# Kernel optimization log

Hardware: AMD Instinct MI355X
Metric: run time of the kernel (lower is better)

## Reference

```python
import jax, jax.numpy as jnp
import numpy as np

FEAT_STRIDE = 16
NEG_OV, POS_OV = 0.3, 0.7
RPN_BATCH = 256
NUM_FG = int(0.5 * RPN_BATCH)  # RPN_FG_FRACTION * RPN_BATCHSIZE


def _gen_anchors(base=16, ratios=(0.5, 1.0, 2.0), scales=(4, 8, 16)):
    # 3D extension of the classic generate_anchors: ratio warps w/h, scale multiplies all dims
    ctr = (base - 1) / 2.0
    rows = []
    for r in ratios:
        for s in scales:
            w = base * s * np.sqrt(1.0 / r)
            h = base * s * np.sqrt(r)
            d = float(base * s)
            rows.append([ctr - 0.5 * (w - 1), ctr - 0.5 * (h - 1),
                         ctr + 0.5 * (w - 1), ctr + 0.5 * (h - 1),
                         ctr - 0.5 * (d - 1), ctr + 0.5 * (d - 1)])
    return np.asarray(rows, np.float32)


def setup_inputs() -> dict:
    key = jax.random.key(0)
    ks = jax.random.split(key, 8)
    B, H, W, D, K, A = 2, 48, 48, 24, 20, 9
    cls = jax.random.normal(ks[0], (B, 2 * A, H, W, D), jnp.float32)
    x1 = jax.random.uniform(ks[1], (B, K)) * 600.0
    y1 = jax.random.uniform(ks[2], (B, K)) * 600.0
    z1 = jax.random.uniform(ks[3], (B, K)) * 300.0
    whd = 16.0 + jax.random.uniform(ks[4], (B, K, 3)) * jnp.array([104.0, 104.0, 48.0])
    x2 = jnp.minimum(x1 + whd[..., 0], 767.0)
    y2 = jnp.minimum(y1 + whd[..., 1], 767.0)
    z2 = jnp.minimum(z1 + whd[..., 2], 383.0)
    cid = jax.random.randint(ks[5], (B, K), 1, 4).astype(jnp.float32)
    gt_boxes = jnp.stack([x1, y1, x2, y2, z1, z2, cid], axis=2)
    im_info = jnp.tile(jnp.array([[768.0, 768.0, 384.0]], jnp.float32), (B, 1))
    total = H * W * D * A
    return {
        'rpn_cls_score': cls,
        'gt_boxes': gt_boxes,
        'im_info': im_info,
        'num_boxes': jnp.full((B,), K, jnp.int32),
        'anchors': jnp.asarray(_gen_anchors()),
        'rand_fg': jax.random.uniform(ks[6], (B, total)),
        'rand_bg': jax.random.uniform(ks[7], (B, total)),
    }


def _overlaps(anc, gt):
    # anc: (N,6) [x1,y1,x2,y2,z1,z2]; gt: (B,K,7) -> IoU (B,N,K)
    aw = anc[:, 2] - anc[:, 0] + 1.0
    ah = anc[:, 3] - anc[:, 1] + 1.0
    ad = anc[:, 5] - anc[:, 4] + 1.0
    a_area = aw * ah * ad  # (N,)
    gw = gt[:, :, 2] - gt[:, :, 0] + 1.0
    gh = gt[:, :, 3] - gt[:, :, 1] + 1.0
    gd = gt[:, :, 5] - gt[:, :, 4] + 1.0
    g_area = gw * gh * gd  # (B,K)
    iw = jnp.clip(jnp.minimum(anc[None, :, None, 2], gt[:, None, :, 2]) -
                  jnp.maximum(anc[None, :, None, 0], gt[:, None, :, 0]) + 1.0, 0.0)
    ih = jnp.clip(jnp.minimum(anc[None, :, None, 3], gt[:, None, :, 3]) -
                  jnp.maximum(anc[None, :, None, 1], gt[:, None, :, 1]) + 1.0, 0.0)
    idp = jnp.clip(jnp.minimum(anc[None, :, None, 5], gt[:, None, :, 5]) -
                   jnp.maximum(anc[None, :, None, 4], gt[:, None, :, 4]) + 1.0, 0.0)
    inter = iw * ih * idp
    ov = inter / (a_area[None, :, None] + g_area[:, None, :] - inter)
    gt_zero = (gw == 1.0) & (gh == 1.0) & (gd == 1.0)
    a_zero = (aw == 1.0) & (ah == 1.0) & (ad == 1.0)
    ov = jnp.where(gt_zero[:, None, :], 0.0, ov)
    ov = jnp.where(a_zero[None, :, None], -1.0, ov)
    return ov


def _transform(ex, gt):
    # ex: (N,6); gt: (B,N,6) -> (B,N,6) targets (dx,dy,dz,dw,dh,dd)
    ew = ex[:, 2] - ex[:, 0] + 1.0
    eh = ex[:, 3] - ex[:, 1] + 1.0
    ed = ex[:, 5] - ex[:, 4] + 1.0
    ecx = ex[:, 0] + 0.5 * (ew - 1.0)
    ecy = ex[:, 1] + 0.5 * (eh - 1.0)
    ecz = ex[:, 4] + 0.5 * (ed - 1.0)
    gw = gt[:, :, 2] - gt[:, :, 0] + 1.0
    gh = gt[:, :, 3] - gt[:, :, 1] + 1.0
    gd = gt[:, :, 5] - gt[:, :, 4] + 1.0
    gcx = gt[:, :, 0] + 0.5 * (gw - 1.0)
    gcy = gt[:, :, 1] + 0.5 * (gh - 1.0)
    gcz = gt[:, :, 4] + 0.5 * (gd - 1.0)
    return jnp.stack([(gcx - ecx[None]) / ew[None],
                      (gcy - ecy[None]) / eh[None],
                      (gcz - ecz[None]) / ed[None],
                      jnp.log(gw / ew[None]),
                      jnp.log(gh / eh[None]),
                      jnp.log(gd / ed[None])], axis=2)


def _rank(p):
    # rank of each element when sorted by descending priority, per row
    return jnp.argsort(jnp.argsort(-p, axis=1), axis=1)


def reference(rpn_cls_score, gt_boxes, im_info, num_boxes, anchors, rand_fg, rand_bg):
    B = gt_boxes.shape[0]
    H, W, D = rpn_cls_score.shape[2], rpn_cls_score.shape[3], rpn_cls_score.shape[4]
    A = anchors.shape[0]
    sx = jnp.arange(W, dtype=jnp.float32) * FEAT_STRIDE
    sy = jnp.arange(H, dtype=jnp.float32) * FEAT_STRIDE
    sz = jnp.arange(D, dtype=jnp.float32) * FEAT_STRIDE
    mx, my, mz = jnp.meshgrid(sx, sy, sz, indexing='xy')  # (H,W,D) each
    shifts = jnp.stack([mx.ravel(), my.ravel(), mx.ravel(), my.ravel(), mz.ravel(), mz.ravel()], axis=1)
    all_anchors = (anchors[None, :, :] + shifts[:, None, :]).reshape(-1, 6)  # (total,6)
    total = all_anchors.shape[0]
    inside = ((all_anchors[:, 0] >= 0) & (all_anchors[:, 1] >= 0) & (all_anchors[:, 4] >= 0) &
              (all_anchors[:, 2] < im_info[0, 1]) & (all_anchors[:, 3] < im_info[0, 0]) &
              (all_anchors[:, 5] < im_info[0, 2]))  # (total,)

    ov = _overlaps(all_anchors, gt_boxes)                       # (B,total,K)
    ov_m = jnp.where(inside[None, :, None], ov, -1.0)           # mask outside anchors
    max_ov = ov_m.max(axis=2)
    argmax_ov = jnp.argmax(ov_m, axis=2)                        # (B,total)

    labels = jnp.full((B, total), -1.0, jnp.float32)
    ins = inside[None, :]
    labels = jnp.where(ins & (max_ov < NEG_OV), 0.0, labels)
    gt_max = ov_m.max(axis=1)                                   # (B,K)
    gt_max = jnp.where(gt_max == 0.0, 1e-5, gt_max)
    tie = jnp.sum(ov_m == gt_max[:, None, :], axis=2) > 0
    labels = jnp.where(ins & tie, 1.0, labels)
    labels = jnp.where(ins & (max_ov >= POS_OV), 1.0, labels)

    # fg subsampling: randomly keep at most NUM_FG positives per image
    fg = labels == 1.0
    rk = _rank(jnp.where(fg, rand_fg, -1.0))
    labels = jnp.where(fg & (rk >= NUM_FG), -1.0, labels)
    # bg subsampling: keep RPN_BATCH - num_fg negatives per image
    num_bg = RPN_BATCH - jnp.sum(labels == 1.0, axis=1)         # (B,)
    bg = labels == 0.0
    rkb = _rank(jnp.where(bg, rand_bg, -1.0))
    labels = jnp.where(bg & (rkb >= num_bg[:, None]), -1.0, labels)

    assigned = jnp.take_along_axis(gt_boxes, argmax_ov[:, :, None], axis=1)  # (B,total,7)
    bbox_targets = _transform(all_anchors, assigned[:, :, :6])
    bbox_targets = jnp.where(inside[None, :, None], bbox_targets, 0.0)

    in_w = jnp.where(labels == 1.0, 1.0, 0.0)                   # RPN_BBOX_INSIDE_WEIGHTS[0]=1
    # replicate original bug: weights from the LAST image's example count
    num_examples = jnp.sum(labels[-1] >= 0.0).astype(jnp.float32)
    w = 1.0 / num_examples
    out_w = jnp.where(labels == 1.0, w, jnp.where(labels == 0.0, w, 0.0))

    labels_o = labels.reshape(B, H, W, D, A).transpose(0, 4, 1, 2, 3).reshape(B, 1, A * H * D, W)
    bt_o = bbox_targets.reshape(B, H, W, D, A * 6).transpose(0, 4, 1, 2, 3)
    iw_o = jnp.broadcast_to(in_w[:, :, None], (B, total, 6)).reshape(B, H, W, D, 6 * A).transpose(0, 4, 1, 2, 3)
    ow_o = jnp.broadcast_to(out_w[:, :, None], (B, total, 6)).reshape(B, H, W, D, 6 * A).transpose(0, 4, 1, 2, 3)
    return labels_o, bt_o, iw_o, ow_o
```

## Files before the change

kernel.cpp:

```cpp
#include <hip/hip_runtime.h>
#include <math.h>

#define BB 2
#define HH 48
#define WW 48
#define DD 24
#define KK 20
#define AA 9
#define TOTAL (HH*WW*DD*AA)
#define SPAT (HH*WW*DD)
#define OUT0N (BB*TOTAL)
#define CH 54
#define NB 4096
#define CAPB 256
#define FG_QUOTA 128
#define RPN_B 256
#define STRIDE_F 16.0f
#define K1_SB 54
#define NPART (AA*K1_SB)

#define O_REC    0
#define O_GTMAX  (OUT0N)
#define O_HIST   (O_GTMAX + BB*KK)
#define O_CUT    (O_HIST + 4*NB)
#define O_W      (O_CUT + 16)
#define O_LIST   (O_W + 1)
#define O_PART   (O_LIST + 4*NB*CAPB)

struct GtRec { float x1,y1,x2,y2,z1,z2,area; };
__device__ __forceinline__ GtRec gt_load(const float* __restrict__ gt, int b, int k){
  #pragma clang fp contract(off)
  const float* p = &gt[(b*KK+k)*7];
  GtRec g;
  g.x1=p[0]; g.y1=p[1]; g.x2=p[2]; g.y2=p[3]; g.z1=p[4]; g.z2=p[5];
  float gw = g.x2-g.x1+1.0f, gh = g.y2-g.y1+1.0f, gd = g.z2-g.z1+1.0f;
  g.area = gw*gh*gd;
  return g;
}

__device__ __forceinline__ float iou_rec(float ax1,float ay1,float ax2,float ay2,
                                         float az1,float az2,float a_area,
                                         const GtRec& g){
  #pragma clang fp contract(off)
  float iw = fminf(ax2,g.x2) - fmaxf(ax1,g.x1) + 1.0f; iw = fmaxf(iw,0.0f);
  float ih = fminf(ay2,g.y2) - fmaxf(ay1,g.y1) + 1.0f; ih = fmaxf(ih,0.0f);
  float id = fminf(az2,g.z2) - fmaxf(az1,g.z1) + 1.0f; id = fmaxf(id,0.0f);
  float inter = iw*ih*id;
  if (inter <= 0.0f) return 0.0f;
  return inter / ((a_area + g.area) - inter);
}

__global__ void __launch_bounds__(256) k_gtmax(const float* __restrict__ gt,
    const float* __restrict__ anc, const float* __restrict__ imi,
    unsigned* __restrict__ ws){
  float* ws_f = (float*)ws;
  __shared__ float s_red[4][KK];
  int tid = threadIdx.x;
  int wv = tid>>6, ln = tid&63;
  int a = blockIdx.y, b = blockIdx.z;
  if (b==0 && a==0 && blockIdx.x<16){
    int base = blockIdx.x*256 + tid;
    #pragma unroll
    for (int j=0;j<4;j++) ws[O_HIST + j*NB + base] = 0u;
  }
  float im0=imi[0], im1=imi[1], im2=imi[2];
  float a0=anc[a*6+0], a1=anc[a*6+1], a2=anc[a*6+2];
  float a3=anc[a*6+3], a4=anc[a*6+4], a5=anc[a*6+5];
  int s0 = blockIdx.x*256 + tid;
  float X1[4],Y1[4],X2[4],Y2[4],Z1[4],Z2[4],AR[4];
  bool OK[4];
  #pragma unroll
  for (int j=0;j<4;j++){
    int s = s0 + j*(K1_SB*256);
    int d = s % DD; int s2 = s/DD; int w = s2%WW; int h = s2/WW;
    float fx=w*STRIDE_F, fy=h*STRIDE_F, fz=d*STRIDE_F;
    X1[j]=a0+fx; Y1[j]=a1+fy; X2[j]=a2+fx; Y2[j]=a3+fy; Z1[j]=a4+fz; Z2[j]=a5+fz;
    OK[j] = (X1[j]>=0.f)&&(Y1[j]>=0.f)&&(Z1[j]>=0.f)&&
            (X2[j]<im1)&&(Y2[j]<im0)&&(Z2[j]<im2);
    {
      #pragma clang fp contract(off)
      float aw=X2[j]-X1[j]+1.0f, ah=Y2[j]-Y1[j]+1.0f, ad=Z2[j]-Z1[j]+1.0f;
      AR[j]=aw*ah*ad;
    }
  }
  #pragma unroll
  for (int k=0;k<KK;k++){
    GtRec g = gt_load(gt,b,k);
    float m = -1.0f;
    #pragma unroll
    for (int j=0;j<4;j++)
      if (OK[j]) m = fmaxf(m, iou_rec(X1[j],Y1[j],X2[j],Y2[j],Z1[j],Z2[j],AR[j],g));
    #pragma unroll
    for (int off=32; off>0; off>>=1) m = fmaxf(m, __shfl_down(m, off, 64));
    if (ln==0) s_red[wv][k]=m;
  }
  __syncthreads();
  if (tid<KK){
    float m = fmaxf(fmaxf(s_red[0][tid],s_red[1][tid]),
                    fmaxf(s_red[2][tid],s_red[3][tid]));
    ws_f[O_PART + (b*KK+tid)*NPART + a*K1_SB + blockIdx.x] = m;
  }
}

__global__ void __launch_bounds__(256) k_label(const float* __restrict__ gt,
    const float* __restrict__ anc, const float* __restrict__ imi,
    const float* __restrict__ rfg, const float* __restrict__ rbg,
    unsigned* __restrict__ ws){
  float* ws_f = (float*)ws;
  __shared__ float s_gm[KK];
  int tid = threadIdx.x;
  int blk = blockIdx.x;
  int wv = tid>>6, ln = tid&63;
  int t4 = (blk*256 + tid)*4;
  int d0 = t4 % DD; int r1=t4/DD; int w=r1%WW; int r2=r1/WW; int h=r2%HH;
  int b = blk/486; int a = (blk%486)/54;
  int ibase = ((h*WW+w)*DD + d0)*AA + a;
  float rfv[4], rbv[4];
  #pragma unroll
  for (int dd=0;dd<4;dd++){
    rfv[dd] = rfg[b*TOTAL + ibase + dd*AA];
    rbv[dd] = rbg[b*TOTAL + ibase + dd*AA];
  }
  for (int k=wv; k<KK; k+=4){
    float m = -1.0f;
    for (int j=ln; j<NPART; j+=64)
      m = fmaxf(m, ws_f[O_PART + (b*KK+k)*NPART + j]);
    #pragma unroll
    for (int off=32; off>0; off>>=1) m = fmaxf(m, __shfl_down(m, off, 64));
    if (ln==0){ if (m==0.0f) m = 1e-5f; s_gm[k]=m; }
  }
  __syncthreads();
  float im0=imi[0], im1=imi[1], im2=imi[2];
  float a0=anc[a*6+0], a1=anc[a*6+1], a2=anc[a*6+2];
  float a3=anc[a*6+3], a4=anc[a*6+4], a5=anc[a*6+5];
  float fx=w*STRIDE_F, fy=h*STRIDE_F;
  float ax1=a0+fx, ay1=a1+fy, ax2=a2+fx, ay2=a3+fy;
  bool okxy = (ax1>=0.f)&&(ay1>=0.f)&&(ax2<im1)&&(ay2<im0);
  float Z1[4],Z2[4],AR[4]; bool OK[4];
  #pragma unroll
  for (int dd=0;dd<4;dd++){
    float fz = (float)(d0+dd)*STRIDE_F;
    Z1[dd]=a4+fz; Z2[dd]=a5+fz;
    OK[dd] = okxy && (Z1[dd]>=0.f) && (Z2[dd]<im2);
    {
      #pragma clang fp contract(off)
      float aw=ax2-ax1+1.0f, ah=ay2-ay1+1.0f, ad=Z2[dd]-Z1[dd]+1.0f;
      AR[dd]=aw*ah*ad;
    }
  }
  float mv[4]={-2.f,-2.f,-2.f,-2.f};
  int   am[4]={0,0,0,0};
  bool  tie[4]={false,false,false,false};
  #pragma unroll
  for (int k=0;k<KK;k++){
    GtRec g = gt_load(gt,b,k);
    float gmk = s_gm[k];
    #pragma unroll
    for (int dd=0;dd<4;dd++){
      if (OK[dd]){
        float ov = iou_rec(ax1,ay1,ax2,ay2,Z1[dd],Z2[dd],AR[dd],g);
        if (ov > mv[dd]){ mv[dd]=ov; am[dd]=k; }
        tie[dd] = tie[dd] || (ov == gmk);
      }
    }
  }
  unsigned recs[4];
  #pragma unroll
  for (int dd=0;dd<4;dd++){
    float L = -1.0f;
    if (OK[dd]){
      if (mv[dd] < 0.3f) L = 0.0f;
      if (tie[dd])       L = 1.0f;
      if (mv[dd] >= 0.7f) L = 1.0f;
    }
    unsigned code = (L==1.0f) ? 2u : ((L==0.0f) ? 1u : 0u);
    unsigned bucket = 0;
    if (code){
      int fl = (code==1u ? 2 : 0) + b;
      float r = (code==1u) ? rbv[dd] : rfv[dd];
      bucket = (unsigned)min(NB-1, (int)(r*(float)NB));
      unsigned pos = atomicAdd(&ws[O_HIST + fl*NB + bucket], 1u);
      if (pos < CAPB) ((int*)ws)[O_LIST + ((fl*NB + (int)bucket)<<8) + pos] = ibase + dd*AA;
    }
    recs[dd] = code | ((unsigned)am[dd]<<2) | (bucket<<7);
  }
  *reinterpret_cast<uint4*>(&ws[O_REC + t4]) = make_uint4(recs[0],recs[1],recs[2],recs[3]);
}

__global__ void __launch_bounds__(256) k_cuts(unsigned* __restrict__ ws){
  int fl = blockIdx.x; int tid = threadIdx.x;
  int b = fl & 1; int isbg = fl >> 1;
  const int CHK = NB/256;
  __shared__ unsigned ps[256];
  __shared__ unsigned s_fg;
  if (tid == 0) s_fg = 0u;
  __syncthreads();
  int hi = NB - CHK*tid;
  unsigned hv[16];
  #pragma unroll
  for (int e=0; e<CHK; e++) hv[e] = ws[O_HIST + fl*NB + (hi-CHK+e)];
  unsigned part = 0;
  #pragma unroll
  for (int e=0; e<CHK; e++) part += hv[e];
  if (isbg){
    unsigned pf = 0;
    #pragma unroll
    for (int e=0; e<CHK; e++) pf += ws[O_HIST + b*NB + tid*CHK + e];
    atomicAdd(&s_fg, pf);
  }
  ps[tid] = part;
  __syncthreads();
  for (int off=1; off<256; off<<=1){
    unsigned v = (tid>=off) ? ps[tid-off] : 0u;
    __syncthreads();
    ps[tid] += v;
    __syncthreads();
  }
  unsigned N = ps[255];
  unsigned excl = ps[tid] - part;
  unsigned F = isbg ? s_fg : N;
  int quota = isbg ? (RPN_B - (int)min(F, (unsigned)FG_QUOTA)) : FG_QUOTA;
  if (fl == 3 && tid == 0){
    int fgk = min((int)F, FG_QUOTA);
    int bgk = min((int)N, RPN_B - fgk);
    ((float*)ws)[O_W] = 1.0f / (float)(fgk + bgk);
  }
  int* cut = (int*)&ws[O_CUT + fl*4];
  if ((int)N <= quota){
    if (tid==0){ cut[0] = -1; cut[1] = 0; cut[2] = quota; cut[3] = 0; }
    return;
  }
  unsigned cum = excl;
  #pragma unroll
  for (int e=CHK-1; e>=0; e--){
    int bk = hi-CHK+e;
    unsigned c = hv[e];
    if (c > 0u && (unsigned)(quota-1) >= cum && (unsigned)(quota-1) < cum + c){
      cut[0] = bk; cut[1] = (int)cum; cut[2] = quota; cut[3] = (int)c;
    }
    cum += c;
  }
}

__global__ void __launch_bounds__(256) k_out(const float* __restrict__ gt,
    const float* __restrict__ anc, const float* __restrict__ imi,
    const float* __restrict__ rfg, const float* __restrict__ rbg,
    float* __restrict__ out, const unsigned* __restrict__ ws){
  __shared__ float s_gt[BB*KK*7];
  __shared__ float s_anc[AA*6];
  __shared__ float s_im[3];
  __shared__ float s_w;
  int tid = threadIdx.x;
  for (int j=tid; j<BB*KK*7; j+=256) s_gt[j] = gt[j];
  for (int j=tid; j<AA*6; j+=256) s_anc[j] = anc[j];
  if (tid<3) s_im[tid] = imi[tid];
  if (tid==0) s_w = ((const float*)ws)[O_W];
  __syncthreads();
  int t4 = (blockIdx.x*256 + tid)*4;
  int d0 = t4 % DD; int r1=t4/DD;
  int w = r1 % WW; int r2 = r1/WW;
  int h = r2 % HH; int r3 = r2/HH;
  int a = r3 % AA; int b = r3/AA;
  const uint4 rec4 = *reinterpret_cast<const uint4*>(&ws[O_REC + t4]);
  unsigned recs[4] = {rec4.x, rec4.y, rec4.z, rec4.w};
  float sw = s_w;
  float fx=w*STRIDE_F, fy=h*STRIDE_F;
  float ax1=s_anc[a*6+0]+fx, ay1=s_anc[a*6+1]+fy;
  float ax2=s_anc[a*6+2]+fx, ay2=s_anc[a*6+3]+fy;
  float L4[4], iw4[4], ow4[4], btv[6][4];
  #pragma unroll
  for (int dd=0; dd<4; dd++){
    int d = d0 + dd;
    unsigned rec = recs[dd];
    unsigned code = rec & 3u;
    int am = (int)((rec>>2) & 31u);
    int bucket = (int)((rec>>7) & 4095u);
    float L = (code==2u) ? 1.0f : ((code==1u) ? 0.0f : -1.0f);
    if (code){
      int isbg = (code==1u);
      int fl = isbg*2 + b;
      const int* cut = (const int*)&ws[O_CUT + fl*4];
      int cutb = cut[0];
      if (cutb >= 0){
        if (bucket < cutb) L = -1.0f;
        else if (bucket == cutb){
          int rank_base = cut[1], quota = cut[2];
          int n = min(cut[3], CAPB);
          int i = ((h*WW+w)*DD + d)*AA + a;
          const float* ra = isbg ? rbg : rfg;
          float ri = ra[b*TOTAL + i];
          const int* lst = (const int*)ws + O_LIST + ((fl*NB + cutb)<<8);
          int cnt = 0;
          for (int e=0; e<n; e++){
            int jj = lst[e];
            float rj = ra[b*TOTAL + jj];
            cnt += (rj > ri) || (rj == ri && jj < i);
          }
          if (rank_base + cnt >= quota) L = -1.0f;
        }
      }
    }
    float fz = d*STRIDE_F;
    float az1 = s_anc[a*6+4]+fz, az2 = s_anc[a*6+5]+fz;
    bool inside = (ax1>=0.f)&&(ay1>=0.f)&&(az1>=0.f)&&
                  (ax2<s_im[1])&&(ay2<s_im[0])&&(az2<s_im[2]);
    float bt[6] = {0.f,0.f,0.f,0.f,0.f,0.f};
    if (inside){
      const float* g = &s_gt[(b*KK + am)*7];
      float ew=ax2-ax1+1.f, eh=ay2-ay1+1.f, ed=az2-az1+1.f;
      float ecx=ax1+0.5f*(ew-1.f), ecy=ay1+0.5f*(eh-1.f), ecz=az1+0.5f*(ed-1.f);
      float gw=g[2]-g[0]+1.f, gh=g[3]-g[1]+1.f, gd=g[5]-g[4]+1.f;
      float gcx=g[0]+0.5f*(gw-1.f), gcy=g[1]+0.5f*(gh-1.f), gcz=g[4]+0.5f*(gd-1.f);
      bt[0]=(gcx-ecx)/ew; bt[1]=(gcy-ecy)/eh; bt[2]=(gcz-ecz)/ed;
      bt[3]=logf(gw/ew);  bt[4]=logf(gh/eh);  bt[5]=logf(gd/ed);
    }
    L4[dd] = L;
    iw4[dd] = (L==1.0f) ? 1.0f : 0.0f;
    ow4[dd] = (L==1.0f || L==0.0f) ? sw : 0.0f;
    #pragma unroll
    for (int c=0; c<6; c++) btv[c][dd] = bt[c];
  }
  *reinterpret_cast<float4*>(&out[t4]) = make_float4(L4[0],L4[1],L4[2],L4[3]);
  int sp = (h*WW + w)*DD + d0;
  float* out1 = out + OUT0N;
  float* out2 = out1 + BB*CH*SPAT;
  float* out3 = out2 + BB*CH*SPAT;
  int basech = (b*CH + a*6)*SPAT + sp;
  float4 iwv = make_float4(iw4[0],iw4[1],iw4[2],iw4[3]);
  float4 owv = make_float4(ow4[0],ow4[1],ow4[2],ow4[3]);
  #pragma unroll
  for (int c=0; c<6; c++){
    int off = basech + c*SPAT;
    *reinterpret_cast<float4*>(&out1[off]) = make_float4(btv[c][0],btv[c][1],btv[c][2],btv[c][3]);
    *reinterpret_cast<float4*>(&out2[off]) = iwv;
    *reinterpret_cast<float4*>(&out3[off]) = owv;
  }
}

extern "C" void kernel_launch(void* const* d_in, const int* in_sizes, int n_in,
                              void* d_out, int out_size, void* d_ws, size_t ws_size,
                              hipStream_t stream) {
  (void)in_sizes; (void)n_in; (void)out_size; (void)ws_size;
  const float* gt  = (const float*)d_in[1];
  const float* imi = (const float*)d_in[2];
  const float* anc = (const float*)d_in[4];
  const float* rfg = (const float*)d_in[5];
  const float* rbg = (const float*)d_in[6];
  float* out = (float*)d_out;
  unsigned* ws = (unsigned*)d_ws;
  int nb4 = (OUT0N + 1023)/1024;
  k_gtmax <<<dim3(K1_SB, AA, BB), dim3(256), 0, stream>>>(gt, anc, imi, ws);
  k_label <<<dim3(nb4), dim3(256), 0, stream>>>(gt, anc, imi, rfg, rbg, ws);
  k_cuts  <<<dim3(4), dim3(256), 0, stream>>>(ws);
  k_out   <<<dim3(nb4), dim3(256), 0, stream>>>(gt, anc, imi, rfg, rbg, out, ws);
}
```

Measured before the change: 189.4 us.

## Fold gt-max reduction and cut computation into last-block epilogues

The per-gt max reduction moves from every k_label block into a last-block-done epilogue of k_gtmax, tracked with an atomic counter. The separate k_cuts launch is folded into the tail of k_label the same way. k_label now handles 2 elements per thread instead of 4, doubling its grid. This removes redundant partial-max rereads and one kernel launch, at the cost of a memset, atomic counters and serialized tail work in a single block.

```diff
diff --git a/kernel.cpp b/kernel.cpp
--- a/kernel.cpp
+++ b/kernel.cpp
@@ -18,6 +18,8 @@
 #define STRIDE_F 16.0f
 #define K1_SB 54
 #define NPART (AA*K1_SB)
+#define K1_GRID (K1_SB*AA*BB)
+#define K2_GRID 1944
 
 #define O_REC    0
 #define O_GTMAX  (OUT0N)
@@ -26,6 +28,7 @@
 #define O_W      (O_CUT + 16)
 #define O_LIST   (O_W + 1)
 #define O_PART   (O_LIST + 4*NB*CAPB)
+#define O_CTR    (O_PART + BB*KK*NPART)
 
 struct GtRec { float x1,y1,x2,y2,z1,z2,area; };
 __device__ __forceinline__ GtRec gt_load(const float* __restrict__ gt, int b, int k){
@@ -50,11 +53,22 @@
   return inter / ((a_area + g.area) - inter);
 }
 
+__device__ __forceinline__ void part_store(float* p, float v){
+  __hip_atomic_store(p, v, __ATOMIC_RELAXED, __HIP_MEMORY_SCOPE_AGENT);
+}
+__device__ __forceinline__ float part_load(const float* p){
+  return __hip_atomic_load(p, __ATOMIC_RELAXED, __HIP_MEMORY_SCOPE_AGENT);
+}
+__device__ __forceinline__ unsigned hist_load(const unsigned* p){
+  return __hip_atomic_load(p, __ATOMIC_RELAXED, __HIP_MEMORY_SCOPE_AGENT);
+}
+
 __global__ void __launch_bounds__(256) k_gtmax(const float* __restrict__ gt,
     const float* __restrict__ anc, const float* __restrict__ imi,
     unsigned* __restrict__ ws){
   float* ws_f = (float*)ws;
   __shared__ float s_red[4][KK];
+  __shared__ bool s_last;
   int tid = threadIdx.x;
   int wv = tid>>6, ln = tid&63;
   int a = blockIdx.y, b = blockIdx.z;
@@ -98,7 +112,24 @@
   if (tid<KK){
     float m = fmaxf(fmaxf(s_red[0][tid],s_red[1][tid]),
                     fmaxf(s_red[2][tid],s_red[3][tid]));
-    ws_f[O_PART + (b*KK+tid)*NPART + a*K1_SB + blockIdx.x] = m;
+    part_store(&ws_f[O_PART + (b*KK+tid)*NPART + a*K1_SB + blockIdx.x], m);
+  }
+  __syncthreads();
+  if (tid==0){
+    __threadfence();
+    s_last = (atomicAdd(&ws[O_CTR+0], 1u) == (unsigned)(K1_GRID-1));
+  }
+  __syncthreads();
+  if (s_last){
+    __threadfence();
+    for (int bk = wv; bk < BB*KK; bk += 4){
+      float m = -1.0f;
+      for (int j=ln; j<NPART; j+=64)
+        m = fmaxf(m, part_load(&ws_f[O_PART + bk*NPART + j]));
+      #pragma unroll
+      for (int off=32; off>0; off>>=1) m = fmaxf(m, __shfl_down(m, off, 64));
+      if (ln==0){ if (m==0.0f) m = 1e-5f; ws_f[O_GTMAX+bk] = m; }
+    }
   }
 }
 
@@ -107,38 +138,31 @@
     const float* __restrict__ rfg, const float* __restrict__ rbg,
     unsigned* __restrict__ ws){
   float* ws_f = (float*)ws;
-  __shared__ float s_gm[KK];
+  __shared__ bool s_last;
   int tid = threadIdx.x;
   int blk = blockIdx.x;
-  int wv = tid>>6, ln = tid&63;
-  int t4 = (blk*256 + tid)*4;
-  int d0 = t4 % DD; int r1=t4/DD; int w=r1%WW; int r2=r1/WW; int h=r2%HH;
-  int b = blk/486; int a = (blk%486)/54;
+  int t2 = (blk*256 + tid)*2;
+  int d0 = t2 % DD; int r1=t2/DD; int w=r1%WW; int r2=r1/WW; int h=r2%HH;
+  int b = blk/972; int a = (blk%972)/108;
   int ibase = ((h*WW+w)*DD + d0)*AA + a;
-  float rfv[4], rbv[4];
-  #pragma unroll
-  for (int dd=0;dd<4;dd++){
+  float rfv[2], rbv[2];
+  #pragma unroll
+  for (int dd=0;dd<2;dd++){
     rfv[dd] = rfg[b*TOTAL + ibase + dd*AA];
     rbv[dd] = rbg[b*TOTAL + ibase + dd*AA];
   }
-  for (int k=wv; k<KK; k+=4){
-    float m = -1.0f;
-    for (int j=ln; j<NPART; j+=64)
-      m = fmaxf(m, ws_f[O_PART + (b*KK+k)*NPART + j]);
-    #pragma unroll
-    for (int off=32; off>0; off>>=1) m = fmaxf(m, __shfl_down(m, off, 64));
-    if (ln==0){ if (m==0.0f) m = 1e-5f; s_gm[k]=m; }
-  }
-  __syncthreads();
+  float gm[KK];
+  #pragma unroll
+  for (int k=0;k<KK;k++) gm[k] = ws_f[O_GTMAX + b*KK + k];
   float im0=imi[0], im1=imi[1], im2=imi[2];
   float a0=anc[a*6+0], a1=anc[a*6+1], a2=anc[a*6+2];
   float a3=anc[a*6+3], a4=anc[a*6+4], a5=anc[a*6+5];
   float fx=w*STRIDE_F, fy=h*STRIDE_F;
   float ax1=a0+fx, ay1=a1+fy, ax2=a2+fx, ay2=a3+fy;
   bool okxy = (ax1>=0.f)&&(ay1>=0.f)&&(ax2<im1)&&(ay2<im0);
-  float Z1[4],Z2[4],AR[4]; bool OK[4];
-  #pragma unroll
-  for (int dd=0;dd<4;dd++){
+  float Z1[2],Z2[2],AR[2]; bool OK[2];
+  #pragma unroll
+  for (int dd=0;dd<2;dd++){
     float fz = (float)(d0+dd)*STRIDE_F;
     Z1[dd]=a4+fz; Z2[dd]=a5+fz;
     OK[dd] = okxy && (Z1[dd]>=0.f) && (Z2[dd]<im2);
@@ -148,15 +172,15 @@
       AR[dd]=aw*ah*ad;
     }
   }
-  float mv[4]={-2.f,-2.f,-2.f,-2.f};
-  int   am[4]={0,0,0,0};
-  bool  tie[4]={false,false,false,false};
+  float mv[2]={-2.f,-2.f};
+  int   am[2]={0,0};
+  bool  tie[2]={false,false};
   #pragma unroll
   for (int k=0;k<KK;k++){
     GtRec g = gt_load(gt,b,k);
-    float gmk = s_gm[k];
-    #pragma unroll
-    for (int dd=0;dd<4;dd++){
+    float gmk = gm[k];
+    #pragma unroll
+    for (int dd=0;dd<2;dd++){
       if (OK[dd]){
         float ov = iou_rec(ax1,ay1,ax2,ay2,Z1[dd],Z2[dd],AR[dd],g);
         if (ov > mv[dd]){ mv[dd]=ov; am[dd]=k; }
@@ -164,9 +188,9 @@
       }
     }
   }
-  unsigned recs[4];
-  #pragma unroll
-  for (int dd=0;dd<4;dd++){
+  unsigned recs[2];
+  #pragma unroll
+  for (int dd=0;dd<2;dd++){
     float L = -1.0f;
     if (OK[dd]){
       if (mv[dd] < 0.3f) L = 0.0f;
@@ -184,61 +208,69 @@
     }
     recs[dd] = code | ((unsigned)am[dd]<<2) | (bucket<<7);
   }
-  *reinterpret_cast<uint4*>(&ws[O_REC + t4]) = make_uint4(recs[0],recs[1],recs[2],recs[3]);
-}
-
-__global__ void __launch_bounds__(256) k_cuts(unsigned* __restrict__ ws){
-  int fl = blockIdx.x; int tid = threadIdx.x;
-  int b = fl & 1; int isbg = fl >> 1;
-  const int CHK = NB/256;
-  __shared__ unsigned ps[256];
-  __shared__ unsigned s_fg;
-  if (tid == 0) s_fg = 0u;
-  __syncthreads();
-  int hi = NB - CHK*tid;
-  unsigned hv[16];
-  #pragma unroll
-  for (int e=0; e<CHK; e++) hv[e] = ws[O_HIST + fl*NB + (hi-CHK+e)];
-  unsigned part = 0;
-  #pragma unroll
-  for (int e=0; e<CHK; e++) part += hv[e];
-  if (isbg){
-    unsigned pf = 0;
-    #pragma unroll
-    for (int e=0; e<CHK; e++) pf += ws[O_HIST + b*NB + tid*CHK + e];
-    atomicAdd(&s_fg, pf);
-  }
-  ps[tid] = part;
-  __syncthreads();
-  for (int off=1; off<256; off<<=1){
-    unsigned v = (tid>=off) ? ps[tid-off] : 0u;
-    __syncthreads();
-    ps[tid] += v;
-    __syncthreads();
-  }
-  unsigned N = ps[255];
-  unsigned excl = ps[tid] - part;
-  unsigned F = isbg ? s_fg : N;
-  int quota = isbg ? (RPN_B - (int)min(F, (unsigned)FG_QUOTA)) : FG_QUOTA;
-  if (fl == 3 && tid == 0){
-    int fgk = min((int)F, FG_QUOTA);
-    int bgk = min((int)N, RPN_B - fgk);
-    ((float*)ws)[O_W] = 1.0f / (float)(fgk + bgk);
-  }
-  int* cut = (int*)&ws[O_CUT + fl*4];
-  if ((int)N <= quota){
-    if (tid==0){ cut[0] = -1; cut[1] = 0; cut[2] = quota; cut[3] = 0; }
-    return;
-  }
-  unsigned cum = excl;
-  #pragma unroll
-  for (int e=CHK-1; e>=0; e--){
-    int bk = hi-CHK+e;
-    unsigned c = hv[e];
-    if (c > 0u && (unsigned)(quota-1) >= cum && (unsigned)(quota-1) < cum + c){
-      cut[0] = bk; cut[1] = (int)cum; cut[2] = quota; cut[3] = (int)c;
-    }
-    cum += c;
+  *reinterpret_cast<uint2*>(&ws[O_REC + t2]) = make_uint2(recs[0],recs[1]);
+  __syncthreads();
+  if (tid==0){
+    __threadfence();
+    s_last = (atomicAdd(&ws[O_CTR+1], 1u) == (unsigned)(K2_GRID-1));
+  }
+  __syncthreads();
+  if (s_last){
+    __threadfence();
+    __shared__ unsigned ps[256];
+    __shared__ unsigned s_fgc;
+    const int CHK = NB/256;
+    for (int fl=0; fl<4; fl++){
+      int bq = fl & 1; int isbg = fl >> 1;
+      if (tid == 0) s_fgc = 0u;
+      __syncthreads();
+      int hi = NB - CHK*tid;
+      unsigned hv[16];
+      #pragma unroll
+      for (int e=0; e<CHK; e++) hv[e] = hist_load(&ws[O_HIST + fl*NB + (hi-CHK+e)]);
+      unsigned part = 0;
+      #pragma unroll
+      for (int e=0; e<CHK; e++) part += hv[e];
+      if (isbg){
+        unsigned pf = 0;
+        #pragma unroll
+        for (int e=0; e<CHK; e++) pf += hist_load(&ws[O_HIST + bq*NB + tid*CHK + e]);
+        atomicAdd(&s_fgc, pf);
+      }
+      ps[tid] = part;
+      __syncthreads();
+      for (int off=1; off<256; off<<=1){
+        unsigned v = (tid>=off) ? ps[tid-off] : 0u;
+        __syncthreads();
+        ps[tid] += v;
+        __syncthreads();
+      }
+      unsigned N = ps[255];
+      unsigned excl = ps[tid] - part;
+      unsigned F = isbg ? s_fgc : N;
+      int quota = isbg ? (RPN_B - (int)min(F, (unsigned)FG_QUOTA)) : FG_QUOTA;
+      if (fl == 3 && tid == 0){
+        int fgk = min((int)F, FG_QUOTA);
+        int bgk = min((int)N, RPN_B - fgk);
+        ws_f[O_W] = 1.0f / (float)(fgk + bgk);
+      }
+      int* cut = (int*)&ws[O_CUT + fl*4];
+      if ((int)N <= quota){
+        if (tid==0){ cut[0] = -1; cut[1] = 0; cut[2] = quota; cut[3] = 0; }
+      } else {
+        unsigned cum = excl;
+        #pragma unroll
+        for (int e=CHK-1; e>=0; e--){
+          int bk = hi-CHK+e;
+          unsigned c = hv[e];
+          if (c > 0u && (unsigned)(quota-1) >= cum && (unsigned)(quota-1) < cum + c){
+            cut[0] = bk; cut[1] = (int)cum; cut[2] = quota; cut[3] = (int)c;
+          }
+          cum += c;
+        }
+      }
+      __syncthreads();
+    }
   }
 }
 
@@ -349,8 +381,8 @@
   float* out = (float*)d_out;
   unsigned* ws = (unsigned*)d_ws;
   int nb4 = (OUT0N + 1023)/1024;
+  hipMemsetAsync((char*)d_ws + (size_t)O_CTR*4, 0, 8, stream);
   k_gtmax <<<dim3(K1_SB, AA, BB), dim3(256), 0, stream>>>(gt, anc, imi, ws);
-  k_label <<<dim3(nb4), dim3(256), 0, stream>>>(gt, anc, imi, rfg, rbg, ws);
-  k_cuts  <<<dim3(4), dim3(256), 0, stream>>>(ws);
+  k_label <<<dim3(K2_GRID), dim3(256), 0, stream>>>(gt, anc, imi, rfg, rbg, ws);
   k_out   <<<dim3(nb4), dim3(256), 0, stream>>>(gt, anc, imi, rfg, rbg, out, ws);
 }
```

Result: slower. 273.2 us (+44.3%).

## Split gt-max reduction into its own kernel and label one anchor per thread

Applied to the files above, without the earlier changes.

Adds a small k_gmfin kernel that reduces the per-block partial IoU maxima to per-gt maxima once, instead of every k_label block redoing that reduction through shared memory. k_label now handles one anchor per thread instead of four, with four times as many blocks, and reads the gt maxima from global memory into registers. The aim is to remove the redundant per-block reduction and to raise parallelism and lower register pressure in the IoU loop. In exchange it adds a kernel launch, replaces vectorized uint4 record stores with scalar stores, and recomputes anchor setup per thread.

```diff
diff --git a/kernel.cpp b/kernel.cpp
--- a/kernel.cpp
+++ b/kernel.cpp
@@ -18,6 +18,7 @@
 #define STRIDE_F 16.0f
 #define K1_SB 54
 #define NPART (AA*K1_SB)
+#define SLABB 216
 
 #define O_REC    0
 #define O_GTMAX  (OUT0N)
@@ -102,89 +103,73 @@
   }
 }
 
+__global__ void __launch_bounds__(64) k_gmfin(unsigned* __restrict__ ws){
+  float* ws_f = (float*)ws;
+  int bk = blockIdx.x;
+  int ln = threadIdx.x;
+  float m = -1.0f;
+  for (int j=ln; j<NPART; j+=64)
+    m = fmaxf(m, ws_f[O_PART + bk*NPART + j]);
+  #pragma unroll
+  for (int off=32; off>0; off>>=1) m = fmaxf(m, __shfl_down(m, off, 64));
+  if (ln==0){ if (m==0.0f) m = 1e-5f; ws_f[O_GTMAX+bk] = m; }
+}
+
 __global__ void __launch_bounds__(256) k_label(const float* __restrict__ gt,
     const float* __restrict__ anc, const float* __restrict__ imi,
     const float* __restrict__ rfg, const float* __restrict__ rbg,
     unsigned* __restrict__ ws){
   float* ws_f = (float*)ws;
-  __shared__ float s_gm[KK];
   int tid = threadIdx.x;
   int blk = blockIdx.x;
-  int wv = tid>>6, ln = tid&63;
-  int t4 = (blk*256 + tid)*4;
-  int d0 = t4 % DD; int r1=t4/DD; int w=r1%WW; int r2=r1/WW; int h=r2%HH;
-  int b = blk/486; int a = (blk%486)/54;
-  int ibase = ((h*WW+w)*DD + d0)*AA + a;
-  float rfv[4], rbv[4];
-  #pragma unroll
-  for (int dd=0;dd<4;dd++){
-    rfv[dd] = rfg[b*TOTAL + ibase + dd*AA];
-    rbv[dd] = rbg[b*TOTAL + ibase + dd*AA];
-  }
-  for (int k=wv; k<KK; k+=4){
-    float m = -1.0f;
-    for (int j=ln; j<NPART; j+=64)
-      m = fmaxf(m, ws_f[O_PART + (b*KK+k)*NPART + j]);
-    #pragma unroll
-    for (int off=32; off>0; off>>=1) m = fmaxf(m, __shfl_down(m, off, 64));
-    if (ln==0){ if (m==0.0f) m = 1e-5f; s_gm[k]=m; }
-  }
-  __syncthreads();
+  int t = blk*256 + tid;
+  int d = t % DD; int r1 = t/DD; int w = r1%WW; int r2 = r1/WW; int h = r2%HH;
+  int slab = blk/SLABB;
+  int a = slab % AA; int b = slab / AA;
+  int i = ((h*WW+w)*DD + d)*AA + a;
+  float rf = rfg[b*TOTAL + i];
+  float rb = rbg[b*TOTAL + i];
+  float gm[KK];
+  #pragma unroll
+  for (int k=0;k<KK;k++) gm[k] = ws_f[O_GTMAX + b*KK + k];
   float im0=imi[0], im1=imi[1], im2=imi[2];
   float a0=anc[a*6+0], a1=anc[a*6+1], a2=anc[a*6+2];
   float a3=anc[a*6+3], a4=anc[a*6+4], a5=anc[a*6+5];
-  float fx=w*STRIDE_F, fy=h*STRIDE_F;
-  float ax1=a0+fx, ay1=a1+fy, ax2=a2+fx, ay2=a3+fy;
-  bool okxy = (ax1>=0.f)&&(ay1>=0.f)&&(ax2<im1)&&(ay2<im0);
-  float Z1[4],Z2[4],AR[4]; bool OK[4];
-  #pragma unroll
-  for (int dd=0;dd<4;dd++){
-    float fz = (float)(d0+dd)*STRIDE_F;
-    Z1[dd]=a4+fz; Z2[dd]=a5+fz;
-    OK[dd] = okxy && (Z1[dd]>=0.f) && (Z2[dd]<im2);
+  float fx=w*STRIDE_F, fy=h*STRIDE_F, fz=d*STRIDE_F;
+  float ax1=a0+fx, ay1=a1+fy, ax2=a2+fx, ay2=a3+fy, az1=a4+fz, az2=a5+fz;
+  bool inside = (ax1>=0.f)&&(ay1>=0.f)&&(az1>=0.f)&&
+                (ax2<im1)&&(ay2<im0)&&(az2<im2);
+  float L = -1.0f;
+  int am = 0;
+  if (inside){
+    float a_area;
     {
       #pragma clang fp contract(off)
-      float aw=ax2-ax1+1.0f, ah=ay2-ay1+1.0f, ad=Z2[dd]-Z1[dd]+1.0f;
-      AR[dd]=aw*ah*ad;
-    }
-  }
-  float mv[4]={-2.f,-2.f,-2.f,-2.f};
-  int   am[4]={0,0,0,0};
-  bool  tie[4]={false,false,false,false};
-  #pragma unroll
-  for (int k=0;k<KK;k++){
-    GtRec g = gt_load(gt,b,k);
-    float gmk = s_gm[k];
-    #pragma unroll
-    for (int dd=0;dd<4;dd++){
-      if (OK[dd]){
-        float ov = iou_rec(ax1,ay1,ax2,ay2,Z1[dd],Z2[dd],AR[dd],g);
-        if (ov > mv[dd]){ mv[dd]=ov; am[dd]=k; }
-        tie[dd] = tie[dd] || (ov == gmk);
-      }
-    }
-  }
-  unsigned recs[4];
-  #pragma unroll
-  for (int dd=0;dd<4;dd++){
-    float L = -1.0f;
-    if (OK[dd]){
-      if (mv[dd] < 0.3f) L = 0.0f;
-      if (tie[dd])       L = 1.0f;
-      if (mv[dd] >= 0.7f) L = 1.0f;
-    }
-    unsigned code = (L==1.0f) ? 2u : ((L==0.0f) ? 1u : 0u);
-    unsigned bucket = 0;
-    if (code){
-      int fl = (code==1u ? 2 : 0) + b;
-      float r = (code==1u) ? rbv[dd] : rfv[dd];
-      bucket = (unsigned)min(NB-1, (int)(r*(float)NB));
-      unsigned pos = atomicAdd(&ws[O_HIST + fl*NB + bucket], 1u);
-      if (pos < CAPB) ((int*)ws)[O_LIST + ((fl*NB + (int)bucket)<<8) + pos] = ibase + dd*AA;
-    }
-    recs[dd] = code | ((unsigned)am[dd]<<2) | (bucket<<7);
-  }
-  *reinterpret_cast<uint4*>(&ws[O_REC + t4]) = make_uint4(recs[0],recs[1],recs[2],recs[3]);
+      float aw=ax2-ax1+1.0f, ah=ay2-ay1+1.0f, ad=az2-az1+1.0f;
+      a_area = aw*ah*ad;
+    }
+    float mv = -2.0f; bool tie = false;
+    #pragma unroll
+    for (int k=0;k<KK;k++){
+      GtRec g = gt_load(gt,b,k);
+      float ov = iou_rec(ax1,ay1,ax2,ay2,az1,az2,a_area,g);
+      if (ov > mv){ mv = ov; am = k; }
+      tie = tie || (ov == gm[k]);
+    }
+    if (mv < 0.3f) L = 0.0f;
+    if (tie)       L = 1.0f;
+    if (mv >= 0.7f) L = 1.0f;
+  }
+  unsigned code = (L==1.0f) ? 2u : ((L==0.0f) ? 1u : 0u);
+  unsigned bucket = 0;
+  if (code){
+    int fl = (code==1u ? 2 : 0) + b;
+    float r = (code==1u) ? rb : rf;
+    bucket = (unsigned)min(NB-1, (int)(r*(float)NB));
+    unsigned pos = atomicAdd(&ws[O_HIST + fl*NB + bucket], 1u);
+    if (pos < CAPB) ((int*)ws)[O_LIST + ((fl*NB + (int)bucket)<<8) + pos] = i;
+  }
+  ws[O_REC + t] = code | ((unsigned)am<<2) | (bucket<<7);
 }
 
 __global__ void __launch_bounds__(256) k_cuts(unsigned* __restrict__ ws){
@@ -348,9 +333,11 @@
   const float* rbg = (const float*)d_in[6];
   float* out = (float*)d_out;
   unsigned* ws = (unsigned*)d_ws;
+  int nb1 = (OUT0N + 255)/256;
   int nb4 = (OUT0N + 1023)/1024;
   k_gtmax <<<dim3(K1_SB, AA, BB), dim3(256), 0, stream>>>(gt, anc, imi, ws);
-  k_label <<<dim3(nb4), dim3(256), 0, stream>>>(gt, anc, imi, rfg, rbg, ws);
+  k_gmfin <<<dim3(BB*KK), dim3(64), 0, stream>>>(ws);
+  k_label <<<dim3(nb1), dim3(256), 0, stream>>>(gt, anc, imi, rfg, rbg, ws);
   k_cuts  <<<dim3(4), dim3(256), 0, stream>>>(ws);
   k_out   <<<dim3(nb4), dim3(256), 0, stream>>>(gt, anc, imi, rfg, rbg, out, ws);
 }
```

New measurement: 174.1 us (median of 2 runs). 8.1% less time.
